# Kernel optimization log

Measured on AMD Instinct MI355X. Metric: run time of the kernel, lower is better.

## Reference

```python
import jax, jax.numpy as jnp
import numpy as np

TEMPERATURE = 1.0
TINY = np.finfo(np.float32).tiny


def setup_inputs() -> dict:
    key = jax.random.key(0)
    ks = jax.random.split(key, 8)
    B, D, H, K, OUT = 2048, 1024, 512, 32, 2
    s = lambda *sh: 1.0 / np.sqrt(sh[0])
    return {
        "x": jax.random.normal(ks[0], (B, D), jnp.float32),
        "uniform": jax.random.uniform(ks[1], (B, K, D), jnp.float32, TINY, 1.0),
        "w0": jax.random.normal(ks[2], (D, H), jnp.float32) * s(D),
        "b0": jnp.zeros((H,), jnp.float32),
        "w1": jax.random.normal(ks[3], (H, H), jnp.float32) * s(H),
        "b1": jnp.zeros((H,), jnp.float32),
        "wout": jax.random.normal(ks[4], (H, D), jnp.float32) * s(H),
        "bout": jnp.zeros((D,), jnp.float32),
        "wp0": jax.random.normal(ks[5], (D, H), jnp.float32) * s(D),
        "bp0": jnp.zeros((H,), jnp.float32),
        "wp1": jax.random.normal(ks[6], (H, OUT), jnp.float32) * s(H),
        "bp1": jnp.zeros((OUT,), jnp.float32),
        "k": K,
    }


def reference(x, uniform, w0, b0, w1, b1, wout, bout, wp0, bp0, wp1, bp1, k):
    # Selector MLP: relu hidden layers, softmax output over the d features.
    h = jax.nn.relu(x @ w0 + b0)
    h = jax.nn.relu(h @ w1 + b1)
    logits = jax.nn.softmax(h @ wout + bout, axis=-1)  # [B, D]

    # create_mask, training branch: Gumbel-softmax concrete relaxation.
    # uniform: [B, K, D]; gumbel = -log(-log(u))
    gumbel = -jnp.log(-jnp.log(uniform))
    noisy = (gumbel + logits[:, None, :]) / TEMPERATURE  # [B, K, D]
    samples = jax.nn.softmax(noisy, axis=-1)
    masks = jnp.max(samples, axis=1)  # [B, D]

    # Predictor MLP on masked inputs (stands in for the saved model).
    new_inputs = x * masks
    hp = jax.nn.relu(new_inputs @ wp0 + bp0)
    deep_out = hp @ wp1 + bp1  # [B, 2]
    return deep_out, masks
```

## Files before the change

kernel.cpp:

```cpp
#include <hip/hip_runtime.h>

#define BB 2048
#define DD 1024
#define HH 512
#define KK 32

#define AS_GLOBAL __attribute__((address_space(1)))
#define AS_LDS    __attribute__((address_space(3)))

typedef __attribute__((ext_vector_type(8))) short short8;
typedef __attribute__((ext_vector_type(4))) float floatx4;

__device__ __forceinline__ float bf2f(unsigned short u) {
    union { unsigned int u; float f; } c; c.u = ((unsigned int)u) << 16; return c.f;
}
__device__ __forceinline__ unsigned short f2bf(float f) {
    union { float f; unsigned int u; } c; c.f = f;
    unsigned int u = c.u + 0x7FFFu + ((c.u >> 16) & 1u);
    return (unsigned short)(u >> 16);
}

#define WOFF_XB    ((size_t)0)
#define WOFF_W0T   ((size_t)4194304)
#define WOFF_W1T   ((size_t)5242880)
#define WOFF_WOUTT ((size_t)5767168)
#define WOFF_WP0T  ((size_t)6815744)
#define WOFF_H0    ((size_t)7864320)
#define WOFF_H1    ((size_t)9961472)
#define WOFF_LG    ((size_t)12058624)
#define WOFF_NEWIN ((size_t)20447232)
#define WOFF_HP    ((size_t)24641536)

__global__ __launch_bounds__(256) void prep_kernel(
    const float* __restrict__ x,  const float* __restrict__ w0,
    const float* __restrict__ w1, const float* __restrict__ wout,
    const float* __restrict__ wp0, unsigned short* __restrict__ ws)
{
    const int blk = blockIdx.x;
    if (blk < 1024) {
        unsigned short* xb = ws + WOFF_XB / 2;
        const size_t base = (size_t)blk * 2048 + (size_t)threadIdx.x * 8;
        float4 v0 = *(const float4*)(x + base);
        float4 v1 = *(const float4*)(x + base + 4);
        ushort4 o0, o1;
        o0.x = f2bf(v0.x); o0.y = f2bf(v0.y); o0.z = f2bf(v0.z); o0.w = f2bf(v0.w);
        o1.x = f2bf(v1.x); o1.y = f2bf(v1.y); o1.z = f2bf(v1.z); o1.w = f2bf(v1.w);
        *(ushort4*)(xb + base) = o0;
        *(ushort4*)(xb + base + 4) = o1;
        return;
    }
    const float* src; unsigned short* dst; int Kd, N, t;
    if (blk < 1536)      { src = w0;   dst = ws + WOFF_W0T / 2;   Kd = 1024; N = 512;  t = blk - 1024; }
    else if (blk < 1792) { src = w1;   dst = ws + WOFF_W1T / 2;   Kd = 512;  N = 512;  t = blk - 1536; }
    else if (blk < 2304) { src = wout; dst = ws + WOFF_WOUTT / 2; Kd = 512;  N = 1024; t = blk - 1792; }
    else                 { src = wp0;  dst = ws + WOFF_WP0T / 2;  Kd = 1024; N = 512;  t = blk - 2304; }
    const int ntn = N / 32;
    const int kt = t / ntn, nt = t % ntn;
    __shared__ float tile[32][33];
    const int tx = threadIdx.x & 31, ty = threadIdx.x >> 5;
#pragma unroll
    for (int r = 0; r < 32; r += 8)
        tile[ty + r][tx] = src[(size_t)(kt * 32 + ty + r) * N + nt * 32 + tx];
    __syncthreads();
#pragma unroll
    for (int r = 0; r < 32; r += 8)
        dst[(size_t)(nt * 32 + ty + r) * Kd + kt * 32 + tx] = f2bf(tile[tx][ty + r]);
}

template <int RELU, int OUTBF>
__global__ __launch_bounds__(256) void gemm_mfma(
    const unsigned short* __restrict__ A,
    const unsigned short* __restrict__ BT,
    const float* __restrict__ bias,
    void* __restrict__ Cv, int M, int N, int Kd)
{
    __shared__ __align__(16) unsigned short As[2][4096];
    __shared__ __align__(16) unsigned short Bs[2][2048];
    const int tid = threadIdx.x;
    const int bm = blockIdx.y * 64, bn = blockIdx.x * 32;
    const int wave = tid >> 6, lane = tid & 63;

    floatx4 acc[2] = {};

    const int sr = tid >> 3;
    const int skc = (tid & 7) ^ ((tid >> 3) & 7);
    const unsigned short* ga  = A  + (size_t)(bm + sr) * Kd + skc * 8;
    const unsigned short* ga2 = ga + (size_t)32 * Kd;
    const unsigned short* gb  = BT + (size_t)(bn + sr) * Kd + skc * 8;
    const int ldoff = wave * 512;

    const int wm = (wave >> 1) * 32, wn = (wave & 1) * 16;
    const int fr = lane & 15, fq = lane >> 4;
    const int e = fr & 7;
    int ua[2];
    ua[0] = (wm + fr) * 8;
    ua[1] = (wm + 16 + fr) * 8;
    const int ub = (wn + fr) * 8;

    const int steps = Kd >> 6;

#define STAGE(buf, k0)                                                              \
    do {                                                                            \
        __builtin_amdgcn_global_load_lds((const AS_GLOBAL void*)(ga + (k0)),        \
            (AS_LDS void*)(&As[buf][0] + ldoff), 16, 0, 0);                         \
        __builtin_amdgcn_global_load_lds((const AS_GLOBAL void*)(ga2 + (k0)),       \
            (AS_LDS void*)(&As[buf][2048] + ldoff), 16, 0, 0);                      \
        __builtin_amdgcn_global_load_lds((const AS_GLOBAL void*)(gb + (k0)),        \
            (AS_LDS void*)(&Bs[buf][0] + ldoff), 16, 0, 0);                         \
    } while (0)

    STAGE(0, 0);
    __syncthreads();

    for (int s = 0; s < steps; ++s) {
        const int buf = s & 1;
        if (s + 1 < steps) STAGE((s + 1) & 1, (s + 1) << 6);
#pragma unroll
        for (int t = 0; t < 2; ++t) {
            const int kc = t * 4 + fq;
            const short8 a0 = *(const short8*)(&As[buf][0] + (size_t)(ua[0] + (kc ^ e)) * 8);
            const short8 a1 = *(const short8*)(&As[buf][0] + (size_t)(ua[1] + (kc ^ e)) * 8);
            const short8 bb = *(const short8*)(&Bs[buf][0] + (size_t)(ub    + (kc ^ e)) * 8);
            acc[0] = __builtin_amdgcn_mfma_f32_16x16x32_bf16(a0, bb, acc[0], 0, 0, 0);
            acc[1] = __builtin_amdgcn_mfma_f32_16x16x32_bf16(a1, bb, acc[1], 0, 0, 0);
        }
        __syncthreads();
    }
#undef STAGE

    float* Cf = (float*)Cv;
    unsigned short* Cb = (unsigned short*)Cv;
    const int er = fq * 4, ec = fr;
    const int col = bn + wn + ec;
    const float bv = bias[col];
#pragma unroll
    for (int i = 0; i < 2; ++i) {
#pragma unroll
        for (int r = 0; r < 4; ++r) {
            const int row = bm + wm + i * 16 + er + r;
            float v = acc[i][r] + bv;
            if (RELU) v = fmaxf(v, 0.0f);
            if (OUTBF) Cb[(size_t)row * N + col] = f2bf(v);
            else       Cf[(size_t)row * N + col] = v;
        }
    }
}

__device__ __forceinline__ float wave_max(float v) {
#pragma unroll
    for (int o = 32; o; o >>= 1) v = fmaxf(v, __shfl_xor(v, o, 64));
    return v;
}
__device__ __forceinline__ float wave_sum(float v) {
#pragma unroll
    for (int o = 32; o; o >>= 1) v += __shfl_xor(v, o, 64);
    return v;
}

__global__ __launch_bounds__(256) void gumbel_fused(
    const float* __restrict__ lgpre,
    const float* __restrict__ uniform,
    const float* __restrict__ x,
    float* __restrict__ masks,
    unsigned short* __restrict__ newin)
{
    const int wave = threadIdx.x >> 6, lane = threadIdx.x & 63;
    const int b = blockIdx.x;
    __shared__ float lmk[4][1024];

    float lp[16];
    const float* lrow = lgpre + (size_t)b * DD;
#pragma unroll
    for (int j = 0; j < 4; ++j)
        *(float4*)(lp + j * 4) = *(const float4*)(lrow + lane * 4 + j * 256);
    float M = -1e30f;
#pragma unroll
    for (int i = 0; i < 16; ++i) M = fmaxf(M, lp[i]);
    M = wave_max(M);
    float S = 0.f;
#pragma unroll
    for (int i = 0; i < 16; ++i) { lp[i] = __expf(lp[i] - M); S += lp[i]; }
    S = wave_sum(S);
    const float invS = 1.0f / S;
    float ep[16];
#pragma unroll
    for (int i = 0; i < 16; ++i) ep[i] = __expf(lp[i] * invS);

    float mk[16] = {0.f,0.f,0.f,0.f,0.f,0.f,0.f,0.f,0.f,0.f,0.f,0.f,0.f,0.f,0.f,0.f};
    const float* up = uniform + (size_t)b * KK * DD + (size_t)wave * DD;
    float4 ucur[4], unext[4];
#pragma unroll
    for (int j = 0; j < 4; ++j)
        ucur[j] = *(const float4*)(up + lane * 4 + j * 256);
    for (int kk = 0; kk < 8; ++kk) {
        if (kk < 7) {
            const float* upn = up + (size_t)(kk + 1) * 4 * DD;
#pragma unroll
            for (int j = 0; j < 4; ++j)
                unext[j] = *(const float4*)(upn + lane * 4 + j * 256);
        }
        float sv[16], sloc = 0.f;
#pragma unroll
        for (int j = 0; j < 4; ++j) {
            const float uu[4] = {ucur[j].x, ucur[j].y, ucur[j].z, ucur[j].w};
#pragma unroll
            for (int q = 0; q < 4; ++q) {
                const float u = uu[q];
                const float vv = u - 1.0f;
                const float tpoly = -vv * (1.4426950f + vv * (-0.7213475f + vv * 0.4808983f));
                const float tlog  = -__builtin_amdgcn_logf(u);
                const float t = (u > 0.984375f) ? tpoly : tlog;
                const float s = ep[j * 4 + q] * __builtin_amdgcn_rcpf(t);
                sv[j * 4 + q] = s;
                sloc += s;
            }
        }
        const float Sk = wave_sum(sloc);
        const float inv = __builtin_amdgcn_rcpf(Sk);
#pragma unroll
        for (int i = 0; i < 16; ++i) mk[i] = fmaxf(mk[i], sv[i] * inv);
#pragma unroll
        for (int j = 0; j < 4; ++j) ucur[j] = unext[j];
    }

#pragma unroll
    for (int j = 0; j < 4; ++j) {
        float4 mo; mo.x = mk[j*4]; mo.y = mk[j*4+1]; mo.z = mk[j*4+2]; mo.w = mk[j*4+3];
        *(float4*)(&lmk[wave][lane * 4 + j * 256]) = mo;
    }
    __syncthreads();
    const int d0 = threadIdx.x * 4;
    const float4 m0 = *(const float4*)(&lmk[0][d0]);
    const float4 m1 = *(const float4*)(&lmk[1][d0]);
    const float4 m2 = *(const float4*)(&lmk[2][d0]);
    const float4 m3 = *(const float4*)(&lmk[3][d0]);
    float4 mm;
    mm.x = fmaxf(fmaxf(m0.x, m1.x), fmaxf(m2.x, m3.x));
    mm.y = fmaxf(fmaxf(m0.y, m1.y), fmaxf(m2.y, m3.y));
    mm.z = fmaxf(fmaxf(m0.z, m1.z), fmaxf(m2.z, m3.z));
    mm.w = fmaxf(fmaxf(m0.w, m1.w), fmaxf(m2.w, m3.w));
    const float4 xv = *(const float4*)(x + (size_t)b * DD + d0);
    *(float4*)(masks + (size_t)b * DD + d0) = mm;
    ushort4 nb;
    nb.x = f2bf(xv.x * mm.x); nb.y = f2bf(xv.y * mm.y);
    nb.z = f2bf(xv.z * mm.z); nb.w = f2bf(xv.w * mm.w);
    *(ushort4*)(newin + (size_t)b * DD + d0) = nb;
}

__global__ __launch_bounds__(256) void final_kernel(
    const unsigned short* __restrict__ hp, const float* __restrict__ wp1,
    const float* __restrict__ bp1, float* __restrict__ out)
{
    const int wave = threadIdx.x >> 6, lane = threadIdx.x & 63;
    const int row = blockIdx.x * 4 + wave;
    const unsigned short* hrow = hp + (size_t)row * HH;
    float a0 = 0.f, a1 = 0.f;
#pragma unroll
    for (int j = 0; j < 8; ++j) {
        const int k = j * 64 + lane;
        const float h = bf2f(hrow[k]);
        const float2 w = *(const float2*)(wp1 + k * 2);
        a0 += h * w.x; a1 += h * w.y;
    }
    a0 = wave_sum(a0); a1 = wave_sum(a1);
    if (lane == 0) {
        out[row * 2 + 0] = a0 + bp1[0];
        out[row * 2 + 1] = a1 + bp1[1];
    }
}

extern "C" void kernel_launch(void* const* d_in, const int* in_sizes, int n_in,
                              void* d_out, int out_size, void* d_ws, size_t ws_size,
                              hipStream_t stream)
{
    (void)in_sizes; (void)n_in; (void)out_size; (void)ws_size;

    const float* x    = (const float*)d_in[0];
    const float* uni  = (const float*)d_in[1];
    const float* w0   = (const float*)d_in[2];
    const float* b0   = (const float*)d_in[3];
    const float* w1   = (const float*)d_in[4];
    const float* b1   = (const float*)d_in[5];
    const float* wout = (const float*)d_in[6];
    const float* bout = (const float*)d_in[7];
    const float* wp0  = (const float*)d_in[8];
    const float* bp0  = (const float*)d_in[9];
    const float* wp1  = (const float*)d_in[10];
    const float* bp1  = (const float*)d_in[11];

    unsigned char* ws = (unsigned char*)d_ws;
    unsigned short* xb    = (unsigned short*)(ws + WOFF_XB);
    unsigned short* w0T   = (unsigned short*)(ws + WOFF_W0T);
    unsigned short* w1T   = (unsigned short*)(ws + WOFF_W1T);
    unsigned short* woutT = (unsigned short*)(ws + WOFF_WOUTT);
    unsigned short* wp0T  = (unsigned short*)(ws + WOFF_WP0T);
    unsigned short* h0    = (unsigned short*)(ws + WOFF_H0);
    unsigned short* h1    = (unsigned short*)(ws + WOFF_H1);
    float*          lg    = (float*)(ws + WOFF_LG);
    unsigned short* newin = (unsigned short*)(ws + WOFF_NEWIN);
    unsigned short* hp    = (unsigned short*)(ws + WOFF_HP);

    float* out   = (float*)d_out;
    float* masks = out + (size_t)BB * 2;

    prep_kernel<<<2816, 256, 0, stream>>>(x, w0, w1, wout, wp0, (unsigned short*)ws);

    gemm_mfma<1, 1><<<dim3(HH / 32, BB / 64), 256, 0, stream>>>(xb, w0T, b0, h0, BB, HH, DD);
    gemm_mfma<1, 1><<<dim3(HH / 32, BB / 64), 256, 0, stream>>>(h0, w1T, b1, h1, BB, HH, HH);
    gemm_mfma<0, 0><<<dim3(DD / 32, BB / 64), 256, 0, stream>>>(h1, woutT, bout, lg, BB, DD, HH);

    gumbel_fused<<<BB, 256, 0, stream>>>(lg, uni, x, masks, newin);

    gemm_mfma<1, 1><<<dim3(HH / 32, BB / 64), 256, 0, stream>>>(newin, wp0T, bp0, hp, BB, HH, DD);
    final_kernel<<<BB / 4, 256, 0, stream>>>(hp, wp1, bp1, out);
}
```

Measured before the change: 435.0 us.

## Fuse final 512->2 projection into predictor GEMM epilogue via atomics

The last predictor GEMM now multiplies its ReLU output by wp1 in the epilogue, reduces across the 16 column lanes with shuffles, and atomically adds the partial dot products into the output. The output is pre-initialized with bp1 by an extra block in the prep kernel. This removes the final kernel launch and the hp intermediate write and read, at the cost of many float atomics and an order-dependent summation. The gumbel kernel also reuses the ucur registers for the scores instead of a separate sv array, to reduce register pressure.

```diff
diff --git a/kernel.cpp b/kernel.cpp
--- a/kernel.cpp
+++ b/kernel.cpp
@@ -29,12 +29,12 @@
 #define WOFF_H1    ((size_t)9961472)
 #define WOFF_LG    ((size_t)12058624)
 #define WOFF_NEWIN ((size_t)20447232)
-#define WOFF_HP    ((size_t)24641536)
 
 __global__ __launch_bounds__(256) void prep_kernel(
     const float* __restrict__ x,  const float* __restrict__ w0,
     const float* __restrict__ w1, const float* __restrict__ wout,
-    const float* __restrict__ wp0, unsigned short* __restrict__ ws)
+    const float* __restrict__ wp0, unsigned short* __restrict__ ws,
+    const float* __restrict__ bp1, float* __restrict__ outp)
 {
     const int blk = blockIdx.x;
     if (blk < 1024) {
@@ -49,6 +49,13 @@
         *(ushort4*)(xb + base + 4) = o1;
         return;
     }
+    if (blk == 2816) {
+        float2 w; w.x = bp1[0]; w.y = bp1[1];
+        float2* o2 = (float2*)outp;
+#pragma unroll
+        for (int r = 0; r < 8; ++r) o2[threadIdx.x * 8 + r] = w;
+        return;
+    }
     const float* src; unsigned short* dst; int Kd, N, t;
     if (blk < 1536)      { src = w0;   dst = ws + WOFF_W0T / 2;   Kd = 1024; N = 512;  t = blk - 1024; }
     else if (blk < 1792) { src = w1;   dst = ws + WOFF_W1T / 2;   Kd = 512;  N = 512;  t = blk - 1536; }
@@ -67,12 +74,14 @@
         dst[(size_t)(nt * 32 + ty + r) * Kd + kt * 32 + tx] = f2bf(tile[tx][ty + r]);
 }
 
-template <int RELU, int OUTBF>
+template <int RELU, int OUTMODE>
 __global__ __launch_bounds__(256) void gemm_mfma(
     const unsigned short* __restrict__ A,
     const unsigned short* __restrict__ BT,
     const float* __restrict__ bias,
-    void* __restrict__ Cv, int M, int N, int Kd)
+    void* __restrict__ Cv, int M, int N, int Kd,
+    const float* __restrict__ wp1o,
+    float* __restrict__ outp)
 {
     __shared__ __align__(16) unsigned short As[2][4096];
     __shared__ __align__(16) unsigned short Bs[2][2048];
@@ -133,6 +142,31 @@
     const int er = fq * 4, ec = fr;
     const int col = bn + wn + ec;
     const float bv = bias[col];
+
+    if (OUTMODE == 2) {
+        const float2 wv = *(const float2*)(wp1o + col * 2);
+#pragma unroll
+        for (int i = 0; i < 2; ++i) {
+#pragma unroll
+            for (int r = 0; r < 4; ++r) {
+                const int row = bm + wm + i * 16 + er + r;
+                float v = acc[i][r] + bv;
+                if (RELU) v = fmaxf(v, 0.0f);
+                float s0 = v * wv.x, s1 = v * wv.y;
+#pragma unroll
+                for (int m = 1; m < 16; m <<= 1) {
+                    s0 += __shfl_xor(s0, m, 64);
+                    s1 += __shfl_xor(s1, m, 64);
+                }
+                if (fr == 0) {
+                    atomicAdd(outp + (size_t)row * 2 + 0, s0);
+                    atomicAdd(outp + (size_t)row * 2 + 1, s1);
+                }
+            }
+        }
+        return;
+    }
+
 #pragma unroll
     for (int i = 0; i < 2; ++i) {
 #pragma unroll
@@ -140,8 +174,8 @@
             const int row = bm + wm + i * 16 + er + r;
             float v = acc[i][r] + bv;
             if (RELU) v = fmaxf(v, 0.0f);
-            if (OUTBF) Cb[(size_t)row * N + col] = f2bf(v);
-            else       Cf[(size_t)row * N + col] = v;
+            if (OUTMODE == 1) Cb[(size_t)row * N + col] = f2bf(v);
+            else              Cf[(size_t)row * N + col] = v;
         }
     }
 }
@@ -199,10 +233,10 @@
             for (int j = 0; j < 4; ++j)
                 unext[j] = *(const float4*)(upn + lane * 4 + j * 256);
         }
-        float sv[16], sloc = 0.f;
+        float sloc = 0.f;
 #pragma unroll
         for (int j = 0; j < 4; ++j) {
-            const float uu[4] = {ucur[j].x, ucur[j].y, ucur[j].z, ucur[j].w};
+            float uu[4] = {ucur[j].x, ucur[j].y, ucur[j].z, ucur[j].w};
 #pragma unroll
             for (int q = 0; q < 4; ++q) {
                 const float u = uu[q];
@@ -211,14 +245,20 @@
                 const float tlog  = -__builtin_amdgcn_logf(u);
                 const float t = (u > 0.984375f) ? tpoly : tlog;
                 const float s = ep[j * 4 + q] * __builtin_amdgcn_rcpf(t);
-                sv[j * 4 + q] = s;
+                uu[q] = s;
                 sloc += s;
             }
+            ucur[j].x = uu[0]; ucur[j].y = uu[1]; ucur[j].z = uu[2]; ucur[j].w = uu[3];
         }
         const float Sk = wave_sum(sloc);
         const float inv = __builtin_amdgcn_rcpf(Sk);
 #pragma unroll
-        for (int i = 0; i < 16; ++i) mk[i] = fmaxf(mk[i], sv[i] * inv);
+        for (int j = 0; j < 4; ++j) {
+            mk[j*4+0] = fmaxf(mk[j*4+0], ucur[j].x * inv);
+            mk[j*4+1] = fmaxf(mk[j*4+1], ucur[j].y * inv);
+            mk[j*4+2] = fmaxf(mk[j*4+2], ucur[j].z * inv);
+            mk[j*4+3] = fmaxf(mk[j*4+3], ucur[j].w * inv);
+        }
 #pragma unroll
         for (int j = 0; j < 4; ++j) ucur[j] = unext[j];
     }
@@ -247,28 +287,6 @@
     *(ushort4*)(newin + (size_t)b * DD + d0) = nb;
 }
 
-__global__ __launch_bounds__(256) void final_kernel(
-    const unsigned short* __restrict__ hp, const float* __restrict__ wp1,
-    const float* __restrict__ bp1, float* __restrict__ out)
-{
-    const int wave = threadIdx.x >> 6, lane = threadIdx.x & 63;
-    const int row = blockIdx.x * 4 + wave;
-    const unsigned short* hrow = hp + (size_t)row * HH;
-    float a0 = 0.f, a1 = 0.f;
-#pragma unroll
-    for (int j = 0; j < 8; ++j) {
-        const int k = j * 64 + lane;
-        const float h = bf2f(hrow[k]);
-        const float2 w = *(const float2*)(wp1 + k * 2);
-        a0 += h * w.x; a1 += h * w.y;
-    }
-    a0 = wave_sum(a0); a1 = wave_sum(a1);
-    if (lane == 0) {
-        out[row * 2 + 0] = a0 + bp1[0];
-        out[row * 2 + 1] = a1 + bp1[1];
-    }
-}
-
 extern "C" void kernel_launch(void* const* d_in, const int* in_sizes, int n_in,
                               void* d_out, int out_size, void* d_ws, size_t ws_size,
                               hipStream_t stream)
@@ -298,19 +316,17 @@
     unsigned short* h1    = (unsigned short*)(ws + WOFF_H1);
     float*          lg    = (float*)(ws + WOFF_LG);
     unsigned short* newin = (unsigned short*)(ws + WOFF_NEWIN);
-    unsigned short* hp    = (unsigned short*)(ws + WOFF_HP);
 
     float* out   = (float*)d_out;
     float* masks = out + (size_t)BB * 2;
 
-    prep_kernel<<<2816, 256, 0, stream>>>(x, w0, w1, wout, wp0, (unsigned short*)ws);
-
-    gemm_mfma<1, 1><<<dim3(HH / 32, BB / 64), 256, 0, stream>>>(xb, w0T, b0, h0, BB, HH, DD);
-    gemm_mfma<1, 1><<<dim3(HH / 32, BB / 64), 256, 0, stream>>>(h0, w1T, b1, h1, BB, HH, HH);
-    gemm_mfma<0, 0><<<dim3(DD / 32, BB / 64), 256, 0, stream>>>(h1, woutT, bout, lg, BB, DD, HH);
+    prep_kernel<<<2817, 256, 0, stream>>>(x, w0, w1, wout, wp0, (unsigned short*)ws, bp1, out);
+
+    gemm_mfma<1, 1><<<dim3(HH / 32, BB / 64), 256, 0, stream>>>(xb, w0T, b0, h0, BB, HH, DD, nullptr, nullptr);
+    gemm_mfma<1, 1><<<dim3(HH / 32, BB / 64), 256, 0, stream>>>(h0, w1T, b1, h1, BB, HH, HH, nullptr, nullptr);
+    gemm_mfma<0, 0><<<dim3(DD / 32, BB / 64), 256, 0, stream>>>(h1, woutT, bout, lg, BB, DD, HH, nullptr, nullptr);
 
     gumbel_fused<<<BB, 256, 0, stream>>>(lg, uni, x, masks, newin);
 
-    gemm_mfma<1, 1><<<dim3(HH / 32, BB / 64), 256, 0, stream>>>(newin, wp0T, bp0, hp, BB, HH, DD);
-    final_kernel<<<BB / 4, 256, 0, stream>>>(hp, wp1, bp1, out);
-}
+    gemm_mfma<1, 2><<<dim3(HH / 32, BB / 64), 256, 0, stream>>>(newin, wp0T, bp0, nullptr, BB, HH, DD, wp1, out);
+}
```

Measured after the change: 437.3 us. About the same (+0.5%).
